# Optimization experiments

Measured on AMD Instinct MI355X. Metric: run time of the kernel, lower is better.

The kernel has to match this reference:

```python
import jax, jax.numpy as jnp
import numpy as np

N_SAMPLES = 32768
N_ATOMS = 1024
ATOM_LEN = 2048
N_TO_KEEP = 1024


def fft_convolve(a, b):
    """Linear convolution via FFT: zero-pad both to 2n, multiply spectra, truncate to n."""
    n = a.shape[-1]
    a = jnp.pad(a, [(0, 0)] * (a.ndim - 1) + [(0, n)])
    b = jnp.pad(b, [(0, 0)] * (b.ndim - 1) + [(0, n)])
    spec = jnp.fft.rfft(a, axis=-1) * jnp.fft.rfft(b, axis=-1)  # broadcast (B,1024,2n//2+1)
    return jnp.fft.irfft(spec, axis=-1)[..., :n]


def sparsify(x, n_to_keep):
    """Keep the top-k raw values over the flattened per-batch feature map; zero the rest."""
    shp = x.shape
    flat = x.reshape(shp[0], -1)                       # (B, 1024*32768)
    vals, idx = jax.lax.top_k(flat, n_to_keep)         # (B, k)
    out = jnp.zeros_like(flat).at[jnp.arange(shp[0])[:, None], idx].set(vals)
    return out.reshape(shp)


def setup_inputs() -> dict:
    key = jax.random.key(0)
    k1, k2 = jax.random.split(key)
    x = jax.random.normal(k1, (2, 1, N_SAMPLES), dtype=jnp.float32)
    # atoms initialized uniform(-0.01, 0.01) in the original module
    atoms = jax.random.uniform(k2, (1, N_ATOMS, ATOM_LEN), dtype=jnp.float32,
                               minval=-0.01, maxval=0.01)
    return {"x": x, "atoms": atoms}


def reference(x, atoms):
    padded = jnp.pad(atoms, ((0, 0), (0, 0), (0, N_SAMPLES - atoms.shape[-1])))  # (1,1024,32768)
    fm = fft_convolve(x, padded)            # (B, 1024, 32768)
    fm = sparsify(fm, N_TO_KEEP)
    recon = fft_convolve(fm, padded)        # (B, 1024, 32768)
    recon = jnp.sum(recon, axis=1, keepdims=True)  # (B, 1, 32768)
    return recon
```

## Files before the change

### kernel.cpp

```cpp
#include <hip/hip_runtime.h>
#include <hip/hip_bf16.h>

#define NS    32768
#define NA    1024
#define AL    2048
#define KKEEP 1024
#define CAPC  (512*1024)

struct Cand { float v; unsigned idx; };

typedef short  short8  __attribute__((ext_vector_type(8)));
typedef short  short4v __attribute__((ext_vector_type(4)));
typedef float  f32x4   __attribute__((ext_vector_type(4)));


__device__ inline unsigned short f2bf(float f) {
    union { float f; unsigned u; } v; v.f = f;
    unsigned r = v.u + 0x7fffu + ((v.u >> 16) & 1u);
    return (unsigned short)(r >> 16);
}

__global__ void prep_kernel(const float* __restrict__ x, const float* __restrict__ atoms,
                            float* __restrict__ hdr, unsigned short* __restrict__ ab16) {
    const int i = blockIdx.x * 256 + threadIdx.x;
    float4 f = *(const float4*)(atoms + (size_t)i * 4);
    ushort4 o;
    o.x = f2bf(f.x); o.y = f2bf(f.y); o.z = f2bf(f.z); o.w = f2bf(f.w);
    *(ushort4*)(ab16 + (size_t)i * 4) = o;
    float sa  = f.x*f.x + f.y*f.y + f.z*f.z + f.w*f.w;
    float sx0 = 0.f, sx1 = 0.f;
    if (i < 16384) {
        float4 xv = *(const float4*)(x + (size_t)i * 4);
        float s = xv.x*xv.x + xv.y*xv.y + xv.z*xv.z + xv.w*xv.w;
        if (i < 8192) sx0 = s; else sx1 = s;
    }
    #pragma unroll
    for (int off = 32; off >= 1; off >>= 1) {
        sa  += __shfl_down(sa , off);
        sx0 += __shfl_down(sx0, off);
        sx1 += __shfl_down(sx1, off);
    }
    if ((threadIdx.x & 63) == 0) {
        atomicAdd(&hdr[2], sa);
        if (sx0 != 0.f) atomicAdd(&hdr[0], sx0);
        if (sx1 != 0.f) atomicAdd(&hdr[1], sx1);
    }
}

#define XRW      2175
#define XRSTRIDE 2192
#define XRB      4384
#define NCPY     4
#define SA_BUF   16384

__device__ inline void gload_lds16(const unsigned short* g, unsigned char* lds) {
    __builtin_amdgcn_global_load_lds((const __attribute__((address_space(1))) void*)g,
                                     (__attribute__((address_space(3))) void*)lds,
                                     16, 0, 0);
}

__global__ __launch_bounds__(256, 3)
void fm_kernel(const float* __restrict__ x, const unsigned short* __restrict__ ab16,
               const float* __restrict__ hdr, unsigned* __restrict__ candCnt,
               Cand* __restrict__ cand, unsigned cap)
{
    __shared__ __align__(16) unsigned char  sA[2 * SA_BUF];
    __shared__ __align__(16) unsigned short sXR[NCPY * XRSTRIDE];

    const int bid = blockIdx.x;
    const int b   = bid >> 11;
    const int rem = bid & 2047;
    const int a0  = (rem >> 8) * 128;
    const int t0  = (rem & 255) * 128;

    const int tid  = threadIdx.x;
    const int lane = tid & 63;
    const int wid  = tid >> 6;
    const int wm   = wid >> 1;
    const int wn   = wid & 1;
    const int g    = lane >> 4;
    const int ln   = lane & 15;

    const int rot = (bid * 5) & 31;

    const float* __restrict__ xb = x + b * NS;

    for (int ti = tid; ti < XRW; ti += 256) {
        int t = t0 - 2047 + ti;
        float f = (t >= 0) ? xb[t] : 0.f;
        unsigned short h = f2bf(f);
        int p0 = 2174 - ti;
        #pragma unroll
        for (int m = 0; m < NCPY; ++m) sXR[m * XRSTRIDE + p0 + m] = h;
    }

    #define STAGE(bf, ck) do {                                                   \
        int kcs = (ck) * 64;                                                     \
        _Pragma("unroll")                                                        \
        for (int it = 0; it < 4; ++it) {                                         \
            int slot = (wid * 4 + it) * 64 + lane;                               \
            int row  = slot >> 3;                                                \
            int blk  = slot & 7;                                                 \
            const unsigned short* gsrc =                                         \
                ab16 + (size_t)(a0 + row) * AL + kcs + ((blk ^ (row & 7)) << 3); \
            gload_lds16(gsrc, sA + (bf) * SA_BUF + (size_t)(wid * 4 + it) * 1024); \
        }                                                                        \
    } while (0)

    f32x4 acc[4][4];
    #pragma unroll
    for (int i = 0; i < 4; ++i)
        #pragma unroll
        for (int j = 0; j < 4; ++j) acc[i][j] = (f32x4)0.0f;

    const int Rbase = 127 - wn * 64 - ln + 8 * g;
    const unsigned char* xrb = (const unsigned char*)sXR;

    int rowoff[4];
    #pragma unroll
    for (int mi = 0; mi < 4; ++mi) rowoff[mi] = (wm * 64 + mi * 16 + ln) * 128;
    const int swz0 = ((0 * 4 + g) ^ (ln & 7)) << 4;
    const int swz1 = ((1 * 4 + g) ^ (ln & 7)) << 4;

    #define LOADB(Rv, dst) do {                                                 \
        int p_ = ((Rv) + 3) & ~3;                                               \
        const unsigned char* a_ =                                               \
            xrb + (unsigned)(p_ - (Rv)) * XRB + (unsigned)p_ * 2u;              \
        short4v lo_ = *(const short4v*)a_;                                      \
        short4v hi_ = *(const short4v*)(a_ + 8);                                \
        dst = __builtin_shufflevector(lo_, hi_, 0, 1, 2, 3, 4, 5, 6, 7);        \
    } while (0)

    short8 b0, b1, b2, b3;

    #define LOADB4(Sv) do {                        \
        LOADB(Rbase      + 32 * (Sv), b0);         \
        LOADB(Rbase - 16 + 32 * (Sv), b1);         \
        LOADB(Rbase - 32 + 32 * (Sv), b2);         \
        LOADB(Rbase - 48 + 32 * (Sv), b3);         \
    } while (0)

    #define ROLLB(Sv) do {                         \
        b3 = b1; b2 = b0;                          \
        LOADB(Rbase      + 32 * (Sv), b0);         \
        LOADB(Rbase - 16 + 32 * (Sv), b1);         \
    } while (0)

    #define MFMAS(mi) do {                                                                  \
        acc[mi][0] = __builtin_amdgcn_mfma_f32_16x16x32_bf16(af[mi], b0, acc[mi][0],0,0,0); \
        acc[mi][1] = __builtin_amdgcn_mfma_f32_16x16x32_bf16(af[mi], b1, acc[mi][1],0,0,0); \
        acc[mi][2] = __builtin_amdgcn_mfma_f32_16x16x32_bf16(af[mi], b2, acc[mi][2],0,0,0); \
        acc[mi][3] = __builtin_amdgcn_mfma_f32_16x16x32_bf16(af[mi], b3, acc[mi][3],0,0,0); \
    } while (0)

    __syncthreads();

    LOADB4(rot * 2);

    STAGE(0, rot);
    STAGE(1, (rot + 1) & 31);

    for (int c = 0; c < 32; ++c) {
        const int chunk  = (c + rot) & 31;
        const int nchunk = (c + 1 + rot) & 31;
        const int cur    = c & 1;

        asm volatile("s_waitcnt vmcnt(4)" ::: "memory");
        __builtin_amdgcn_sched_barrier(0);
        __builtin_amdgcn_s_barrier();
        __builtin_amdgcn_sched_barrier(0);

        #pragma unroll
        for (int s = 0; s < 2; ++s) {
            short8 af[4];
            const int soff = cur * SA_BUF + (s ? swz1 : swz0);
            #pragma unroll
            for (int mi = 0; mi < 4; ++mi)
                af[mi] = *(const short8*)(sA + soff + rowoff[mi]);

            __builtin_amdgcn_s_setprio(1);
            MFMAS(0); MFMAS(1); MFMAS(2); MFMAS(3);
            __builtin_amdgcn_s_setprio(0);

            if (s == 0) {
                ROLLB(chunk * 2 + 1);
            } else {
                if (nchunk == 0) { LOADB4(0); }
                else             { ROLLB(nchunk * 2); }
            }
        }

        __builtin_amdgcn_sched_barrier(0);
        __builtin_amdgcn_s_barrier();
        __builtin_amdgcn_sched_barrier(0);

        STAGE(cur, (c + 2 + rot) & 31);
    }
    #undef LOADB
    #undef LOADB4
    #undef ROLLB
    #undef MFMAS
    #undef STAGE

    const float sig = sqrtf((hdr[2] * (1.0f / (float)NA)) * (hdr[b] * (1.0f / (float)NS)));
    const float T0  = 3.70f * sig;

    #pragma unroll
    for (int mi = 0; mi < 4; ++mi) {
        #pragma unroll
        for (int ni = 0; ni < 4; ++ni) {
            #pragma unroll
            for (int r = 0; r < 4; ++r) {
                float v = acc[mi][ni][r];
                if (v > T0) {
                    unsigned a = (unsigned)(a0 + wm * 64 + mi * 16 + g * 4 + r);
                    unsigned t = (unsigned)(t0 + wn * 64 + ni * 16 + ln);
                    unsigned idx = (a << 15) | t;
                    unsigned pos = atomicAdd(&candCnt[b], 1u);
                    if (pos < cap) {
                        Cand cc; cc.v = v; cc.idx = idx;
                        cand[(size_t)b * cap + pos] = cc;
                    }
                }
            }
        }
    }
}

__global__ void refine_band(const float* __restrict__ x, const float* __restrict__ atoms,
                            const float* __restrict__ hdr,
                            const unsigned* __restrict__ candCnt, Cand* __restrict__ cand,
                            unsigned cap) {
    const int lane = threadIdx.x & 63;
    const int wv   = (int)((blockIdx.x * blockDim.x + threadIdx.x) >> 6);
    const int nw   = (int)((gridDim.x * blockDim.x) >> 6);
    const int n0 = (int)min(candCnt[0], cap);
    const int n1 = (int)min(candCnt[1], cap);
    const int total = n0 + n1;
    for (int c = wv; c < total; c += nw) {
        const int b = (c < n0) ? 0 : 1;
        const size_t ci = (c < n0) ? (size_t)c : ((size_t)cap + (size_t)(c - n0));
        const float sig = sqrtf((hdr[2] * (1.0f / (float)NA)) * (hdr[b] * (1.0f / (float)NS)));
        const Cand cc = cand[ci];
        if (cc.v <= 3.85f * sig) continue;
        const unsigned idx = cc.idx;
        const int a = (int)(idx >> 15);
        const int t = (int)(idx & (NS - 1));
        const float* __restrict__ ar = atoms + (size_t)a * AL;
        const float* __restrict__ xr = x + b * NS;
        double s = 0.0;
        for (int k = lane; k < AL; k += 64) {
            int xi = t - k;
            if (xi >= 0) s += (double)ar[k] * (double)xr[xi];
        }
        #pragma unroll
        for (int o = 32; o >= 1; o >>= 1) s += __shfl_down(s, o);
        if (lane == 0) cand[ci].v = (float)s;
    }
}

#define SELCAP 16384

__global__ void select_kernel(const unsigned* __restrict__ candCnt,
                              const Cand* __restrict__ cand, Cand* __restrict__ sel,
                              unsigned cap) {
    __shared__ float    s_vals[SELCAP];
    __shared__ float    s_red[16];
    __shared__ int      s_cnt;
    __shared__ int      s_nA;
    __shared__ int      s_nT;
    __shared__ int      s_exact;
    __shared__ float    s_tau;
    __shared__ Cand     s_A[KKEEP];
    __shared__ unsigned s_T[256];

    const int b = blockIdx.x;
    const Cand* __restrict__ cb = cand + (size_t)b * cap;
    const int n   = (int)min(candCnt[b], cap);
    const int tid = threadIdx.x;

    if (n <= KKEEP) {
        for (int i = tid; i < KKEEP; i += blockDim.x) {
            Cand z; z.v = 0.f; z.idx = 0u;
            sel[b * KKEEP + i] = (i < n) ? cb[i] : z;
        }
        return;
    }

    const bool useLds = (n <= SELCAP);
    if (useLds)
        for (int i = tid; i < n; i += blockDim.x) s_vals[i] = cb[i].v;

    float m = 0.f;
    if (useLds) { __syncthreads();
        for (int i = tid; i < n; i += blockDim.x) m = fmaxf(m, s_vals[i]);
    } else {
        for (int i = tid; i < n; i += blockDim.x) m = fmaxf(m, cb[i].v);
    }
    #pragma unroll
    for (int o = 32; o >= 1; o >>= 1) m = fmaxf(m, __shfl_down(m, o));
    if ((tid & 63) == 0) s_red[tid >> 6] = m;
    if (tid == 0) s_exact = 0;
    __syncthreads();
    float hi;
    {
        float mm = 0.f;
        #pragma unroll
        for (int w = 0; w < 16; ++w) mm = fmaxf(mm, s_red[w]);
        hi = mm;
    }
    float lo = 0.f;
    for (int iter = 0; iter < 64; ++iter) {
        float mid = 0.5f * (lo + hi);
        if (!(mid > lo && mid < hi)) break;
        if (tid == 0) s_cnt = 0;
        __syncthreads();
        int c = 0;
        if (useLds) for (int i = tid; i < n; i += blockDim.x) c += (s_vals[i] > mid) ? 1 : 0;
        else        for (int i = tid; i < n; i += blockDim.x) c += (cb[i].v  > mid) ? 1 : 0;
        #pragma unroll
        for (int o = 32; o >= 1; o >>= 1) c += __shfl_down(c, o);
        if ((tid & 63) == 0) atomicAdd(&s_cnt, c);
        __syncthreads();
        int cm = s_cnt;
        __syncthreads();
        if (cm == KKEEP) { if (tid == 0) { s_tau = mid; s_exact = 1; } break; }
        if (cm > KKEEP) lo = mid; else hi = mid;
    }
    __syncthreads();

    const int   exact = s_exact;
    const float tau   = exact ? s_tau : hi;

    for (int i = tid; i < KKEEP; i += blockDim.x) { s_A[i].v = 0.f; s_A[i].idx = 0u; }
    if (tid == 0) { s_nA = 0; s_nT = 0; }
    __syncthreads();

    for (int i = tid; i < n; i += blockDim.x) {
        float v = cb[i].v;
        if (v > tau) {
            int p = atomicAdd(&s_nA, 1);
            if (p < KKEEP) s_A[p] = cb[i];
        } else if (!exact && v == tau) {
            int p = atomicAdd(&s_nT, 1);
            if (p < 256) s_T[p] = cb[i].idx;
        }
    }
    __syncthreads();
    if (tid == 0) {
        int nA = s_nA; if (nA > KKEEP) nA = KKEEP;
        int need = KKEEP - nA;
        int nT = s_nT; if (nT > 256) nT = 256;
        for (int r = 0; r < need && r < nT; ++r) {
            unsigned best = 0xffffffffu; int bj = -1;
            for (int j = 0; j < nT; ++j) if (s_T[j] < best) { best = s_T[j]; bj = j; }
            Cand c; c.v = tau; c.idx = best;
            s_A[nA + r] = c;
            if (bj >= 0) s_T[bj] = 0xffffffffu;
        }
    }
    __syncthreads();
    for (int i = tid; i < KKEEP; i += blockDim.x) sel[b * KKEEP + i] = s_A[i];
}

__global__ void recon_kernel(const float* __restrict__ atoms, const Cand* __restrict__ sel,
                             float* __restrict__ out) {
    __shared__ float s_cv[KKEEP];
    __shared__ int   s_ca[KKEEP];
    __shared__ int   s_ct[KKEEP];
    __shared__ int   s_n;
    const int b    = blockIdx.x >> 7;
    const int tseg = (blockIdx.x & 127) << 8;
    const int t    = tseg + threadIdx.x;
    if (threadIdx.x == 0) s_n = 0;
    __syncthreads();
    for (int i = threadIdx.x; i < KKEEP; i += blockDim.x) {
        Cand c = sel[b * KKEEP + i];
        int t0e = (int)(c.idx & (NS - 1));
        if (c.v != 0.f && t0e <= tseg + 255 && t0e + (AL - 1) >= tseg) {
            int p = atomicAdd(&s_n, 1);
            s_cv[p] = c.v;
            s_ca[p] = (int)(c.idx >> 15);
            s_ct[p] = t0e;
        }
    }
    __syncthreads();
    const int n = s_n;
    float acc = 0.f;
    for (int e = 0; e < n; ++e) {
        int d = t - s_ct[e];
        if ((unsigned)d < (unsigned)AL)
            acc += s_cv[e] * atoms[(size_t)s_ca[e] * AL + d];
    }
    out[b * NS + t] = acc;
}

extern "C" void kernel_launch(void* const* d_in, const int* in_sizes, int n_in,
                              void* d_out, int out_size, void* d_ws, size_t ws_size,
                              hipStream_t stream) {
    const float* x     = (const float*)d_in[0];
    const float* atoms = (const float*)d_in[1];
    float* out = (float*)d_out;

    float*          hdr     = (float*)d_ws;
    unsigned*       candCnt = (unsigned*)((char*)d_ws + 16);
    Cand*           sel     = (Cand*)((char*)d_ws + 64);
    unsigned short* ab16    = (unsigned short*)((char*)d_ws + 65536);
    const size_t    candOff = 65536 + (size_t)NA * AL * 2;
    Cand*           cand    = (Cand*)((char*)d_ws + candOff);

    unsigned cap = CAPC;
    if (ws_size > candOff + 2 * sizeof(Cand) * 1024) {
        size_t fit = (ws_size - candOff) / (2 * sizeof(Cand));
        if (fit < cap) cap = (unsigned)fit;
    } else {
        cap = 1024;
    }

    hipMemsetAsync(d_ws, 0, 256, stream);
    prep_kernel  <<<(NA * AL) / (256 * 4), 256, 0, stream>>>(x, atoms, hdr, ab16);
    fm_kernel    <<<2 * (NA / 128) * (NS / 128), 256, 0, stream>>>(x, ab16, hdr, candCnt, cand, cap);
    refine_band  <<<512, 256, 0, stream>>>(x, atoms, hdr, candCnt, cand, cap);
    select_kernel<<<2, 1024, 0, stream>>>(candCnt, cand, sel, cap);
    recon_kernel <<<256, 256, 0, stream>>>(atoms, sel, out);
}
```

Measured before the change: 437.9 us.

## Fuse refine pass into fm kernel and replace memset/atomics with per-block partial sums

Drops the hipMemsetAsync and the separate refine_band launch. prep_kernel now writes per-block partial sums of squared norms and zeroes the candidate counters, replacing the global float atomics. Each fm block reduces all 2048 partials to get the threshold, queues its above-band candidates in LDS, and recomputes them in double precision right after the GEMM. This removes two launches and the extra pass over candidates. In exchange every fm block re-reads the 24 KB partial-sum array, and the per-block queue is capped at 64 entries, so any band candidates beyond that are not refined.

Measured after the change: 473.6 us. +8.2%, slower.

```diff
diff --git a/kernel.cpp b/kernel.cpp
--- a/kernel.cpp
+++ b/kernel.cpp
@@ -21,8 +21,12 @@
 }
 
 __global__ void prep_kernel(const float* __restrict__ x, const float* __restrict__ atoms,
-                            float* __restrict__ hdr, unsigned short* __restrict__ ab16) {
-    const int i = blockIdx.x * 256 + threadIdx.x;
+                            float* __restrict__ psum, unsigned* __restrict__ candCnt,
+                            unsigned short* __restrict__ ab16) {
+    __shared__ float red[12];
+    const int bid = blockIdx.x;
+    const int tid = threadIdx.x;
+    const int i   = bid * 256 + tid;
     float4 f = *(const float4*)(atoms + (size_t)i * 4);
     ushort4 o;
     o.x = f2bf(f.x); o.y = f2bf(f.y); o.z = f2bf(f.z); o.w = f2bf(f.w);
@@ -40,10 +44,17 @@
         sx0 += __shfl_down(sx0, off);
         sx1 += __shfl_down(sx1, off);
     }
-    if ((threadIdx.x & 63) == 0) {
-        atomicAdd(&hdr[2], sa);
-        if (sx0 != 0.f) atomicAdd(&hdr[0], sx0);
-        if (sx1 != 0.f) atomicAdd(&hdr[1], sx1);
+    if ((tid & 63) == 0) {
+        red[(tid >> 6) * 3 + 0] = sa;
+        red[(tid >> 6) * 3 + 1] = sx0;
+        red[(tid >> 6) * 3 + 2] = sx1;
+    }
+    __syncthreads();
+    if (tid == 0) {
+        psum[bid * 3 + 0] = red[0] + red[3] + red[6] + red[9];
+        psum[bid * 3 + 1] = red[1] + red[4] + red[7] + red[10];
+        psum[bid * 3 + 2] = red[2] + red[5] + red[8] + red[11];
+        if (bid == 0) { candCnt[0] = 0u; candCnt[1] = 0u; }
     }
 }
 
@@ -60,12 +71,17 @@
 }
 
 __global__ __launch_bounds__(256, 3)
-void fm_kernel(const float* __restrict__ x, const unsigned short* __restrict__ ab16,
-               const float* __restrict__ hdr, unsigned* __restrict__ candCnt,
+void fm_kernel(const float* __restrict__ x, const float* __restrict__ af32,
+               const unsigned short* __restrict__ ab16,
+               const float* __restrict__ psum, unsigned* __restrict__ candCnt,
                Cand* __restrict__ cand, unsigned cap)
 {
     __shared__ __align__(16) unsigned char  sA[2 * SA_BUF];
     __shared__ __align__(16) unsigned short sXR[NCPY * XRSTRIDE];
+    __shared__ float    sred[12];
+    __shared__ unsigned bq_pos[64];
+    __shared__ unsigned bq_idx[64];
+    __shared__ int      bq_n;
 
     const int bid = blockIdx.x;
     const int b   = bid >> 11;
@@ -202,8 +218,32 @@
     #undef MFMAS
     #undef STAGE
 
-    const float sig = sqrtf((hdr[2] * (1.0f / (float)NA)) * (hdr[b] * (1.0f / (float)NS)));
-    const float T0  = 3.70f * sig;
+    if (tid == 0) bq_n = 0;
+    float pa = 0.f, p0s = 0.f, p1s = 0.f;
+    for (int j = tid; j < 2048; j += 256) {
+        pa  += psum[3 * j + 0];
+        p0s += psum[3 * j + 1];
+        p1s += psum[3 * j + 2];
+    }
+    #pragma unroll
+    for (int o = 32; o >= 1; o >>= 1) {
+        pa  += __shfl_down(pa , o);
+        p0s += __shfl_down(p0s, o);
+        p1s += __shfl_down(p1s, o);
+    }
+    if ((tid & 63) == 0) {
+        sred[(tid >> 6) * 3 + 0] = pa;
+        sred[(tid >> 6) * 3 + 1] = p0s;
+        sred[(tid >> 6) * 3 + 2] = p1s;
+    }
+    __syncthreads();
+    const float SA = sred[0] + sred[3] + sred[6] + sred[9];
+    const float S0 = sred[1] + sred[4] + sred[7] + sred[10];
+    const float S1 = sred[2] + sred[5] + sred[8] + sred[11];
+    const float sig = sqrtf((SA * (1.0f / (float)NA)) *
+                            (((b == 0) ? S0 : S1) * (1.0f / (float)NS)));
+    const float T0 = 3.70f * sig;
+    const float TB = 3.85f * sig;
 
     #pragma unroll
     for (int mi = 0; mi < 4; ++mi) {
@@ -220,42 +260,32 @@
                     if (pos < cap) {
                         Cand cc; cc.v = v; cc.idx = idx;
                         cand[(size_t)b * cap + pos] = cc;
+                        if (v > TB) {
+                            int q = atomicAdd(&bq_n, 1);
+                            if (q < 64) { bq_pos[q] = pos; bq_idx[q] = idx; }
+                        }
                     }
                 }
             }
         }
     }
-}
-
-__global__ void refine_band(const float* __restrict__ x, const float* __restrict__ atoms,
-                            const float* __restrict__ hdr,
-                            const unsigned* __restrict__ candCnt, Cand* __restrict__ cand,
-                            unsigned cap) {
-    const int lane = threadIdx.x & 63;
-    const int wv   = (int)((blockIdx.x * blockDim.x + threadIdx.x) >> 6);
-    const int nw   = (int)((gridDim.x * blockDim.x) >> 6);
-    const int n0 = (int)min(candCnt[0], cap);
-    const int n1 = (int)min(candCnt[1], cap);
-    const int total = n0 + n1;
-    for (int c = wv; c < total; c += nw) {
-        const int b = (c < n0) ? 0 : 1;
-        const size_t ci = (c < n0) ? (size_t)c : ((size_t)cap + (size_t)(c - n0));
-        const float sig = sqrtf((hdr[2] * (1.0f / (float)NA)) * (hdr[b] * (1.0f / (float)NS)));
-        const Cand cc = cand[ci];
-        if (cc.v <= 3.85f * sig) continue;
-        const unsigned idx = cc.idx;
-        const int a = (int)(idx >> 15);
-        const int t = (int)(idx & (NS - 1));
-        const float* __restrict__ ar = atoms + (size_t)a * AL;
-        const float* __restrict__ xr = x + b * NS;
+    __syncthreads();
+
+    int nq = bq_n; if (nq > 64) nq = 64;
+    for (int e = wid; e < nq; e += 4) {
+        const unsigned ie = bq_idx[e];
+        const unsigned pe = bq_pos[e];
+        const int aa = (int)(ie >> 15);
+        const int tt = (int)(ie & (NS - 1));
+        const float* __restrict__ ar = af32 + (size_t)aa * AL;
         double s = 0.0;
         for (int k = lane; k < AL; k += 64) {
-            int xi = t - k;
-            if (xi >= 0) s += (double)ar[k] * (double)xr[xi];
+            int xi = tt - k;
+            if (xi >= 0) s += (double)ar[k] * (double)xb[xi];
         }
         #pragma unroll
         for (int o = 32; o >= 1; o >>= 1) s += __shfl_down(s, o);
-        if (lane == 0) cand[ci].v = (float)s;
+        if (lane == 0) cand[(size_t)b * cap + pe].v = (float)s;
     }
 }
 
@@ -402,9 +432,9 @@
     const float* atoms = (const float*)d_in[1];
     float* out = (float*)d_out;
 
-    float*          hdr     = (float*)d_ws;
-    unsigned*       candCnt = (unsigned*)((char*)d_ws + 16);
-    Cand*           sel     = (Cand*)((char*)d_ws + 64);
+    unsigned*       candCnt = (unsigned*)d_ws;
+    float*          psum    = (float*)((char*)d_ws + 64);
+    Cand*           sel     = (Cand*)((char*)d_ws + 32768);
     unsigned short* ab16    = (unsigned short*)((char*)d_ws + 65536);
     const size_t    candOff = 65536 + (size_t)NA * AL * 2;
     Cand*           cand    = (Cand*)((char*)d_ws + candOff);
@@ -417,10 +447,8 @@
         cap = 1024;
     }
 
-    hipMemsetAsync(d_ws, 0, 256, stream);
-    prep_kernel  <<<(NA * AL) / (256 * 4), 256, 0, stream>>>(x, atoms, hdr, ab16);
-    fm_kernel    <<<2 * (NA / 128) * (NS / 128), 256, 0, stream>>>(x, ab16, hdr, candCnt, cand, cap);
-    refine_band  <<<512, 256, 0, stream>>>(x, atoms, hdr, candCnt, cand, cap);
+    prep_kernel  <<<2048, 256, 0, stream>>>(x, atoms, psum, candCnt, ab16);
+    fm_kernel    <<<2 * (NA / 128) * (NS / 128), 256, 0, stream>>>(x, atoms, ab16, psum, candCnt, cand, cap);
     select_kernel<<<2, 1024, 0, stream>>>(candCnt, cand, sel, cap);
     recon_kernel <<<256, 256, 0, stream>>>(atoms, sel, out);
 }
```
